# Kernel optimization log

Measured on AMD Instinct MI355X. Metric: run time of the kernel, lower is better.

The kernel has to match this reference:

```python
import jax, jax.numpy as jnp
import numpy as np

DIM = 16      # must equal K*K per the module's reshape structure
K = 4         # kernel_size
HEADS = 8
SCALE = (DIM // HEADS) ** (-0.5)


def setup_inputs() -> dict:
    key = jax.random.key(0)
    k1, k2 = jax.random.split(key)
    x = jax.random.normal(k1, (2, 64, 67, 67), dtype=jnp.float32)
    # torch Linear(dim, 3*dim, bias=False) weight: [3*dim, dim]
    w_qkv = jax.random.normal(k2, (3 * DIM, DIM), dtype=jnp.float32) * 0.1
    return {"x": x, "w_qkv": w_qkv}


def reference(x, w_qkv):
    B, C, H, W = x.shape
    k = K
    Ho, Wo = H - k + 1, W - k + 1          # unfold output grid (stride=1)
    L = Ho * Wo
    # Unfold: patches[b, c, i*k+j, ph, pw] = x[b, c, ph+i, pw+j]
    # (matches torch F.unfold channel ordering c-major, then i, then j)
    patches = jnp.stack(
        [x[:, :, i:i + Ho, j:j + Wo] for i in range(k) for j in range(k)],
        axis=2,
    )  # [B, C, k*k, Ho, Wo]
    seq = L // (k * k)                      # L must be divisible by k*k
    # [B*C*k*k, seq, k*k] -- flatten (Ho,Wo)->L row-major then split into (seq, k*k)
    xu = patches.reshape(B * C * k * k, seq, k * k)
    # tiny attention over each row; feature dim = k*k = DIM
    qkv = xu @ w_qkv.T                      # [N, seq, 3*DIM]
    q, kk_, v = jnp.split(qkv, 3, axis=-1)
    scores = jnp.einsum('nqd,nkd->nqk', q, kk_) * SCALE   # [N, seq, seq]
    attn = jax.nn.softmax(scores, axis=-1)                # dropout = identity (eval)
    ao = jnp.einsum('nqk,nkd->nqd', attn, v)              # [N, seq, DIM]
    ao = ao.reshape(B, C, k, k, Ho, Wo)
    # overlap-add fold back onto the HxW grid
    out = jnp.zeros_like(x)
    for i in range(k):
        for j in range(k):
            out = out.at[:, :, i:Ho + i, j:Wo + j].add(ao[:, :, i, j])
    return out
```

## Files before the change

### kernel.cpp

```cpp
#include <hip/hip_runtime.h>


#define BATCH 2
#define CHAN 64
#define HWDIM 67
#define SEQ 256
#define DIM 16
#define NSEQ 2048
#define PLANE 4096
#define OUT_TOTAL (BATCH * CHAN * HWDIM * HWDIM)
#define ATT_SCALE 0.70710678118654752f
#define LOG2E 1.44269504088896340736f
#define HTILES 17

typedef _Float16 half4 __attribute__((ext_vector_type(4)));
typedef _Float16 half8 __attribute__((ext_vector_type(8)));
typedef float float4v __attribute__((ext_vector_type(4)));
typedef __fp16 fp16x2 __attribute__((ext_vector_type(2)));
typedef unsigned int uint2v __attribute__((ext_vector_type(2)));

static __device__ __forceinline__ half4 mk_half4(float a, float b, float c, float d) {
    fp16x2 lo = __builtin_amdgcn_cvt_pkrtz(a, b);
    fp16x2 hi = __builtin_amdgcn_cvt_pkrtz(c, d);
    uint2v u;
    u[0] = __builtin_bit_cast(unsigned int, lo);
    u[1] = __builtin_bit_cast(unsigned int, hi);
    return __builtin_bit_cast(half4, u);
}

static __device__ __forceinline__ half4 pack4(float4v c) {
    return mk_half4(c[0], c[1], c[2], c[3]);
}

__global__ __launch_bounds__(512, 4) void ska_attn_pass1(
    const float* __restrict__ x,
    const float* __restrict__ w,
    _Float16* __restrict__ ao)
{
    __shared__ __align__(16) _Float16 buf[2][16][64][8];

    const int half_id = threadIdx.x >> 8;
    const int n  = blockIdx.x * 2 + half_id;
    const int p  = n & 15;
    const int bc = n >> 4;
    const int oi = p >> 2;
    const int oj = p & 3;

    const int s   = threadIdx.x & 255;
    const int ph  = s >> 2;
    const int pw0 = (s & 3) * DIM;

    const float* xrow = x + ((size_t)bc * HWDIM + (ph + oi)) * HWDIM + pw0 + oj;
    const int kt = s >> 4, kk = s & 15;
#pragma unroll
    for (int dh = 0; dh < 4; ++dh) {
        const half4 h = mk_half4(xrow[4 * dh + 0], xrow[4 * dh + 1],
                                 xrow[4 * dh + 2], xrow[4 * dh + 3]);
        *(half4*)&buf[half_id][kt][kk + 16 * dh][0] = h;
    }

    const int wave = (threadIdx.x >> 6) & 3;
    const int lane = threadIdx.x & 63;
    const int o = lane & 15;
    const int g = lane >> 4;

    const float4 wq4 = *(const float4*)(w + ( 0 + o) * DIM + 4 * g);
    const float4 wk4 = *(const float4*)(w + (16 + o) * DIM + 4 * g);
    const float4 wv4 = *(const float4*)(w + (32 + o) * DIM + 4 * g);
    const half4 wqf = mk_half4(wq4.x * (ATT_SCALE * LOG2E), wq4.y * (ATT_SCALE * LOG2E),
                               wq4.z * (ATT_SCALE * LOG2E), wq4.w * (ATT_SCALE * LOG2E));
    const half4 wkf = mk_half4(wk4.x, wk4.y, wk4.z, wk4.w);
    const half4 wvf = mk_half4(wv4.x, wv4.y, wv4.z, wv4.w);

    const float4v zf = (float4v){0.f, 0.f, 0.f, 0.f};

    half4 qfr[4];
#pragma unroll
    for (int u = 0; u < 4; ++u) {
        const int t = 4 * wave + u;
        const half4 xf = *(const half4*)&buf[half_id][t][lane][0];
        const half4 kf = pack4(__builtin_amdgcn_mfma_f32_16x16x16f16(wkf, xf, zf, 0, 0, 0));
        const half4 vf = pack4(__builtin_amdgcn_mfma_f32_16x16x16f16(xf, wvf, zf, 0, 0, 0));
        const half8 kv = __builtin_shufflevector(kf, vf, 0, 1, 2, 3, 4, 5, 6, 7);
        *(half8*)&buf[half_id][t][lane][0] = kv;
        qfr[u] = pack4(__builtin_amdgcn_mfma_f32_16x16x16f16(wqf, xf, zf, 0, 0, 0));
    }
    __syncthreads();

    float4v oacc[4];
    float lpart[4];
#pragma unroll
    for (int j = 0; j < 4; ++j) {
        oacc[j] = zf;
        lpart[j] = 0.f;
    }

#pragma unroll 4
    for (int t = 0; t < 16; ++t) {
        const half8 kv = *(const half8*)&buf[half_id][t][lane][0];
        const half4 kf = __builtin_shufflevector(kv, kv, 0, 1, 2, 3);
        const half4 vf = __builtin_shufflevector(kv, kv, 4, 5, 6, 7);
#pragma unroll
        for (int j = 0; j < 4; ++j) {
            float4v sfr = __builtin_amdgcn_mfma_f32_16x16x16f16(kf, qfr[j], zf, 0, 0, 0);
            const float p0 = __builtin_amdgcn_exp2f(sfr[0]);
            const float p1 = __builtin_amdgcn_exp2f(sfr[1]);
            const float p2 = __builtin_amdgcn_exp2f(sfr[2]);
            const float p3 = __builtin_amdgcn_exp2f(sfr[3]);
            lpart[j] += (p0 + p1) + (p2 + p3);
            const half4 pb = mk_half4(p0, p1, p2, p3);
            oacc[j] = __builtin_amdgcn_mfma_f32_16x16x16f16(vf, pb, oacc[j], 0, 0, 0);
        }
    }

#pragma unroll
    for (int j = 0; j < 4; ++j) {
        float lj = lpart[j];
        lj += __shfl_xor(lj, 16, 64);
        lj += __shfl_xor(lj, 32, 64);
        const float rl = 1.f / lj;
        const int query = (4 * wave + j) * 16 + (lane & 15);
        const half4 hv = mk_half4(oacc[j][0] * rl, oacc[j][1] * rl,
                                  oacc[j][2] * rl, oacc[j][3] * rl);
        *(half4*)(ao + (size_t)n * PLANE + query * DIM + 4 * g) = hv;
    }
}

__global__ __launch_bounds__(256) void ska_fold_pass2(
    const _Float16* __restrict__ ao,
    float* __restrict__ out)
{
    __shared__ __align__(16) _Float16 sA[16][4][64];

    const int blk = blockIdx.x;
    const int h0  = (blk % HTILES) * 4;
    const int bc  = blk / HTILES;
    const int tid = threadIdx.x;

    {
        const int pl = tid >> 4;
        const int hh = (tid >> 2) & 3;
        const int pw = (tid & 3) * 16;
        const int i  = pl >> 2;
        const int prow = h0 + hh - i;
        half8 v0, v1;
        if (prow >= 0 && prow < 64) {
            const _Float16* src = ao + ((size_t)(bc * 16 + pl)) * PLANE + prow * 64 + pw;
            v0 = *(const half8*)src;
            v1 = *(const half8*)(src + 8);
        } else {
            const half8 z = (half8)(_Float16)0.f;
            v0 = z; v1 = z;
        }
        *(half8*)&sA[pl][hh][pw]     = v0;
        *(half8*)&sA[pl][hh][pw + 8] = v1;
    }
    __syncthreads();

    for (int px = tid; px < 4 * HWDIM; px += 256) {
        const int hh = px / HWDIM;
        const int ww = px % HWDIM;
        const int h  = h0 + hh;
        if (h >= HWDIM) continue;
        float acc = 0.f;
#pragma unroll
        for (int i = 0; i < 4; ++i) {
#pragma unroll
            for (int j = 0; j < 4; ++j) {
                const int pw = ww - j;
                if (pw < 0 || pw >= 64) continue;
                acc += (float)sA[i * 4 + j][hh][pw];
            }
        }
        out[((size_t)bc * HWDIM + h) * HWDIM + ww] = acc;
    }
}

__global__ __launch_bounds__(256) void ska_attn_atomic(
    const float* __restrict__ x, const float* __restrict__ w,
    float* __restrict__ out)
{
    __shared__ float sw[3 * DIM * DIM];
    __shared__ float sk[SEQ][DIM];
    __shared__ float sv[SEQ][DIM];

    const int n = blockIdx.x, p = n & 15, bc = n >> 4, oi = p >> 2, oj = p & 3;
    const int s = threadIdx.x, ph = s >> 2, pw0 = (s & 3) * DIM;

#pragma unroll
    for (int r = 0; r < 3; ++r) sw[r * 256 + s] = w[r * 256 + s];

    const float* xrow = x + ((size_t)bc * HWDIM + (ph + oi)) * HWDIM + pw0 + oj;
    float xr[DIM];
#pragma unroll
    for (int d = 0; d < DIM; ++d) xr[d] = xrow[d];
    __syncthreads();

    float q[DIM];
#pragma unroll
    for (int o = 0; o < DIM; ++o) {
        float aq = 0.f, ak = 0.f, av = 0.f;
#pragma unroll
        for (int d = 0; d < DIM; ++d) {
            aq += xr[d] * sw[o * DIM + d];
            ak += xr[d] * sw[(DIM + o) * DIM + d];
            av += xr[d] * sw[(2 * DIM + o) * DIM + d];
        }
        q[o] = aq * ATT_SCALE; sk[s][o] = ak; sv[s][o] = av;
    }
    __syncthreads();

    float l = 0.f, acc[DIM];
#pragma unroll
    for (int d = 0; d < DIM; ++d) acc[d] = 0.f;
    for (int t = 0; t < SEQ; ++t) {
        float sc = 0.f;
#pragma unroll
        for (int d = 0; d < DIM; ++d) sc += q[d] * sk[t][d];
        const float pe = __expf(sc);
        l += pe;
#pragma unroll
        for (int d = 0; d < DIM; ++d) acc[d] += pe * sv[t][d];
    }
    const float rl = 1.f / l;
    float* obase = out + ((size_t)bc * HWDIM + (ph + oi)) * HWDIM + pw0 + oj;
#pragma unroll
    for (int d = 0; d < DIM; ++d) atomicAdd(&obase[d], acc[d] * rl);
}

extern "C" void kernel_launch(void* const* d_in, const int* in_sizes, int n_in,
                              void* d_out, int out_size, void* d_ws, size_t ws_size,
                              hipStream_t stream) {
    const float* x = (const float*)d_in[0];
    const float* w = (const float*)d_in[1];
    float* out = (float*)d_out;

    const size_t need = (size_t)NSEQ * PLANE * sizeof(_Float16);
    if (ws_size >= need) {
        _Float16* ao = (_Float16*)d_ws;
        ska_attn_pass1<<<NSEQ / 2, 512, 0, stream>>>(x, w, ao);
        ska_fold_pass2<<<BATCH * CHAN * HTILES, 256, 0, stream>>>(ao, out);
    } else {
        (void)hipMemsetAsync(out, 0, (size_t)out_size * sizeof(float), stream);
        ska_attn_atomic<<<NSEQ, 256, 0, stream>>>(x, w, out);
    }
}
```

Baseline: 85.15 us.

## Process four sequences per block with two waves each and batched MFMA groups

Pass 1 now handles four sequences per 512-thread block, two waves per sequence, so each wave owns 8 query tiles instead of 4. The per-sequence K/V fragment loaded from shared memory is reused across twice as many queries. The inner loop is fully unrolled and regrouped so four score MFMAs issue together, then four exp blocks, then four PV MFMAs, which lets MFMA latency overlap with the transcendental work. In exchange, register pressure rises (8 accumulators plus 8 query fragments), shared memory per block doubles, and the grid halves, which may lower occupancy.

```diff
diff --git a/kernel.cpp b/kernel.cpp
--- a/kernel.cpp
+++ b/kernel.cpp
@@ -37,30 +37,34 @@
     const float* __restrict__ w,
     _Float16* __restrict__ ao)
 {
-    __shared__ __align__(16) _Float16 buf[2][16][64][8];
-
-    const int half_id = threadIdx.x >> 8;
-    const int n  = blockIdx.x * 2 + half_id;
+    __shared__ __align__(16) _Float16 buf[4][16][64][8];
+
+    const int tid   = threadIdx.x;
+    const int sid   = tid >> 7;
+    const int lane  = tid & 63;
+    const int qhalf = (tid >> 6) & 1;
+
+    const int n  = blockIdx.x * 4 + sid;
     const int p  = n & 15;
     const int bc = n >> 4;
     const int oi = p >> 2;
     const int oj = p & 3;
 
-    const int s   = threadIdx.x & 255;
-    const int ph  = s >> 2;
-    const int pw0 = (s & 3) * DIM;
-
-    const float* xrow = x + ((size_t)bc * HWDIM + (ph + oi)) * HWDIM + pw0 + oj;
-    const int kt = s >> 4, kk = s & 15;
+    const int tok0 = qhalf * 128 + 2 * lane;
+    const int kt   = tok0 >> 4;
+    const int kk0  = tok0 & 15;
+    const float* xrow = x + ((size_t)bc * HWDIM + (tok0 >> 2) + oi) * HWDIM
+                          + (tok0 & 3) * DIM + oj;
 #pragma unroll
     for (int dh = 0; dh < 4; ++dh) {
-        const half4 h = mk_half4(xrow[4 * dh + 0], xrow[4 * dh + 1],
-                                 xrow[4 * dh + 2], xrow[4 * dh + 3]);
-        *(half4*)&buf[half_id][kt][kk + 16 * dh][0] = h;
-    }
-
-    const int wave = (threadIdx.x >> 6) & 3;
-    const int lane = threadIdx.x & 63;
+        const half4 h0 = mk_half4(xrow[4 * dh + 0],  xrow[4 * dh + 1],
+                                  xrow[4 * dh + 2],  xrow[4 * dh + 3]);
+        const half4 h1 = mk_half4(xrow[16 + 4 * dh + 0], xrow[16 + 4 * dh + 1],
+                                  xrow[16 + 4 * dh + 2], xrow[16 + 4 * dh + 3]);
+        *(half4*)&buf[sid][kt][kk0     + 16 * dh][0] = h0;
+        *(half4*)&buf[sid][kt][kk0 + 1 + 16 * dh][0] = h1;
+    }
+
     const int o = lane & 15;
     const int g = lane >> 4;
 
@@ -74,52 +78,61 @@
 
     const float4v zf = (float4v){0.f, 0.f, 0.f, 0.f};
 
-    half4 qfr[4];
-#pragma unroll
-    for (int u = 0; u < 4; ++u) {
-        const int t = 4 * wave + u;
-        const half4 xf = *(const half4*)&buf[half_id][t][lane][0];
+    half4 qfr[8];
+#pragma unroll
+    for (int u = 0; u < 8; ++u) {
+        const int t = 8 * qhalf + u;
+        const half4 xf = *(const half4*)&buf[sid][t][lane][0];
         const half4 kf = pack4(__builtin_amdgcn_mfma_f32_16x16x16f16(wkf, xf, zf, 0, 0, 0));
         const half4 vf = pack4(__builtin_amdgcn_mfma_f32_16x16x16f16(xf, wvf, zf, 0, 0, 0));
         const half8 kv = __builtin_shufflevector(kf, vf, 0, 1, 2, 3, 4, 5, 6, 7);
-        *(half8*)&buf[half_id][t][lane][0] = kv;
+        *(half8*)&buf[sid][t][lane][0] = kv;
         qfr[u] = pack4(__builtin_amdgcn_mfma_f32_16x16x16f16(wqf, xf, zf, 0, 0, 0));
     }
     __syncthreads();
 
-    float4v oacc[4];
-    float lpart[4];
-#pragma unroll
-    for (int j = 0; j < 4; ++j) {
+    float4v oacc[8];
+    float lpart[8];
+#pragma unroll
+    for (int j = 0; j < 8; ++j) {
         oacc[j] = zf;
         lpart[j] = 0.f;
     }
 
-#pragma unroll 4
+#pragma unroll
     for (int t = 0; t < 16; ++t) {
-        const half8 kv = *(const half8*)&buf[half_id][t][lane][0];
+        const half8 kv = *(const half8*)&buf[sid][t][lane][0];
         const half4 kf = __builtin_shufflevector(kv, kv, 0, 1, 2, 3);
         const half4 vf = __builtin_shufflevector(kv, kv, 4, 5, 6, 7);
 #pragma unroll
-        for (int j = 0; j < 4; ++j) {
-            float4v sfr = __builtin_amdgcn_mfma_f32_16x16x16f16(kf, qfr[j], zf, 0, 0, 0);
-            const float p0 = __builtin_amdgcn_exp2f(sfr[0]);
-            const float p1 = __builtin_amdgcn_exp2f(sfr[1]);
-            const float p2 = __builtin_amdgcn_exp2f(sfr[2]);
-            const float p3 = __builtin_amdgcn_exp2f(sfr[3]);
-            lpart[j] += (p0 + p1) + (p2 + p3);
-            const half4 pb = mk_half4(p0, p1, p2, p3);
-            oacc[j] = __builtin_amdgcn_mfma_f32_16x16x16f16(vf, pb, oacc[j], 0, 0, 0);
-        }
-    }
-
-#pragma unroll
-    for (int j = 0; j < 4; ++j) {
+        for (int grp = 0; grp < 2; ++grp) {
+            float4v sfr[4];
+#pragma unroll
+            for (int u = 0; u < 4; ++u)
+                sfr[u] = __builtin_amdgcn_mfma_f32_16x16x16f16(kf, qfr[4 * grp + u], zf, 0, 0, 0);
+            half4 pb[4];
+#pragma unroll
+            for (int u = 0; u < 4; ++u) {
+                const float p0 = __builtin_amdgcn_exp2f(sfr[u][0]);
+                const float p1 = __builtin_amdgcn_exp2f(sfr[u][1]);
+                const float p2 = __builtin_amdgcn_exp2f(sfr[u][2]);
+                const float p3 = __builtin_amdgcn_exp2f(sfr[u][3]);
+                lpart[4 * grp + u] += (p0 + p1) + (p2 + p3);
+                pb[u] = mk_half4(p0, p1, p2, p3);
+            }
+#pragma unroll
+            for (int u = 0; u < 4; ++u)
+                oacc[4 * grp + u] = __builtin_amdgcn_mfma_f32_16x16x16f16(vf, pb[u], oacc[4 * grp + u], 0, 0, 0);
+        }
+    }
+
+#pragma unroll
+    for (int j = 0; j < 8; ++j) {
         float lj = lpart[j];
         lj += __shfl_xor(lj, 16, 64);
         lj += __shfl_xor(lj, 32, 64);
         const float rl = 1.f / lj;
-        const int query = (4 * wave + j) * 16 + (lane & 15);
+        const int query = (8 * qhalf + j) * 16 + (lane & 15);
         const half4 hv = mk_half4(oacc[j][0] * rl, oacc[j][1] * rl,
                                   oacc[j][2] * rl, oacc[j][3] * rl);
         *(half4*)(ao + (size_t)n * PLANE + query * DIM + 4 * g) = hv;
@@ -238,7 +251,7 @@
     const size_t need = (size_t)NSEQ * PLANE * sizeof(_Float16);
     if (ws_size >= need) {
         _Float16* ao = (_Float16*)d_ws;
-        ska_attn_pass1<<<NSEQ / 2, 512, 0, stream>>>(x, w, ao);
+        ska_attn_pass1<<<NSEQ / 4, 512, 0, stream>>>(x, w, ao);
         ska_fold_pass2<<<BATCH * CHAN * HTILES, 256, 0, stream>>>(ao, out);
     } else {
         (void)hipMemsetAsync(out, 0, (size_t)out_size * sizeof(float), stream);
```

After: 96.86 us. +13.8%, slower.
